# Kernel optimization log

Hardware: AMD Instinct MI355X
Metric: run time of the kernel (lower is better)

## Reference

```python
import jax, jax.numpy as jnp
import numpy as np
from jax import lax

N_FFT = 512
HOP = 128
Q = N_FFT // HOP  # 4
KW = 2 * N_FFT - 1  # conv kernel width 1023


def _hann_periodic(n: int) -> np.ndarray:
    # scipy.signal.get_window('hann', n) default fftbins=True -> periodic hann
    k = np.arange(n)
    return (0.5 - 0.5 * np.cos(2.0 * np.pi * k / n)).astype(np.float64)


def _compute_alpha(W: np.ndarray, S: np.ndarray) -> np.ndarray:
    # Faithful port of ConsistencyLoss._compute_alpha (paper eq. 9)
    N, R = N_FFT, HOP
    alpha = np.zeros((2 * Q - 1, 2 * N - 1), dtype=np.complex64)
    for qi, q in enumerate(range(-(Q - 1), Q)):
        S_sh = np.zeros(N)
        s0, s1 = max(0, -q * R), min(N, N - q * R)
        if s0 < s1:
            S_sh[s0:s1] = S[q * R + s0: q * R + s1]
        term = W * S_sh
        f = np.fft.fft(term, 2 * N - 1)
        alpha[qi] = np.fft.fftshift(f) / N
    alpha[Q - 1, N - 1] -= 1.0
    return alpha


def setup_inputs() -> dict:
    key = jax.random.key(0)
    waveform = 0.1 * jax.random.normal(key, (4, 131072), dtype=jnp.float32)
    W_np = _hann_periodic(N_FFT)
    alpha = _compute_alpha(W_np, W_np)
    return {
        "waveform": waveform,
        "window": jnp.asarray(W_np, dtype=jnp.float32),
        "alpha_real": jnp.asarray(alpha.real, dtype=jnp.float32),
        "alpha_imag": jnp.asarray(alpha.imag, dtype=jnp.float32),
    }


def _stft(waveform, window):
    # torch.stft(center=True, pad_mode='reflect', onesided=True), output (B, T, F)
    N, hop = N_FFT, HOP
    B, L = waveform.shape
    padded = jnp.pad(waveform, ((0, 0), (N // 2, N // 2)), mode="reflect")
    T = 1 + L // hop
    idx = hop * jnp.arange(T)[:, None] + jnp.arange(N)[None, :]  # (T, N)
    frames = padded[:, idx] * window  # (B, T, N)
    return jnp.fft.rfft(frames, axis=-1)  # (B, T, N//2+1) complex64


def reference(waveform, window, alpha_real, alpha_imag):
    N, hop = N_FFT, HOP
    B = waveform.shape[0]
    H = _stft(waveform, window)  # (B, T, N//2+1)
    T = H.shape[1]

    # reconstruct full two-sided spectrum: concat conj-flipped interior bins
    H_full = jnp.concatenate([H, jnp.conj(H[:, :, 1:-1][:, :, ::-1])], axis=2)  # (B, T, N)
    H_full = jnp.transpose(H_full, (0, 2, 1))  # (B, N, T)

    # fuse the phase-term einsum into the per-frequency conv kernel:
    # C[b,n,t] = sum_q phase[n,q] * (alpha[q] * H_full[b,n])(t)
    #          = (K_eff[n] * H_full[b,n])(t),  K_eff = phase @ alpha
    q_idx = jnp.arange(-(Q - 1), Q, dtype=jnp.float32)
    n_idx = jnp.arange(N, dtype=jnp.float32)
    phase = jnp.exp(1j * (2.0 * jnp.pi / N) * n_idx[:, None] * q_idx[None, :])  # (N, 2Q-1)
    alpha = alpha_real + 1j * alpha_imag  # (2Q-1, KW)
    K = phase @ alpha.astype(jnp.complex64)  # (N, KW)
    Kr, Ki = jnp.real(K), jnp.imag(K)

    # complex depthwise (groups=N) cross-correlation via real 2-channel trick
    Hri = jnp.stack([jnp.real(H_full), jnp.imag(H_full)], axis=2).reshape(B, 2 * N, T)
    kern = jnp.stack([
        jnp.stack([Kr, -Ki], axis=1),  # real output rows (N, 2, KW)
        jnp.stack([Ki, Kr], axis=1),   # imag output rows (N, 2, KW)
    ], axis=1).reshape(2 * N, 2, KW)
    out = lax.conv_general_dilated(
        Hri, kern, window_strides=(1,), padding=[(N - 1, N - 1)],
        dimension_numbers=("NCH", "OIH", "NCH"), feature_group_count=N,
    )  # (B, 2N, T)
    Cr, Ci = out[:, 0::2], out[:, 1::2]  # (B, N, T)

    loss = jnp.sum(Cr * Cr + Ci * Ci)
    return loss / (B * T)
```

## Files before the change

### kernel.cpp

```cpp
#include <hip/hip_runtime.h>
#include <math.h>

#define T_FRAMES 1025
#define TSTRIDE  1032
#define BATCH    4
#define LWAV     131072
#define KWC      1023
#define MFFT     2048
#define PI_F     3.14159265358979323846f

struct c32 { float r, i; };
__device__ __forceinline__ c32 mkc(float r, float i){ c32 z; z.r=r; z.i=i; return z; }
__device__ __forceinline__ c32 cadd(c32 a, c32 b){ return mkc(a.r+b.r, a.i+b.i); }
__device__ __forceinline__ c32 csub(c32 a, c32 b){ return mkc(a.r-b.r, a.i-b.i); }
__device__ __forceinline__ c32 cmul(c32 a, c32 b){ return mkc(a.r*b.r - a.i*b.i, a.r*b.i + a.i*b.r); }
__device__ __forceinline__ c32 cni(c32 a){ return mkc(a.i, -a.r); }
#define C8F 0.70710678118654752440f
__device__ __forceinline__ c32 c8p(c32 a){ return mkc(C8F*(a.r+a.i), C8F*(a.i-a.r)); }
__device__ __forceinline__ c32 c8m(c32 a){ return mkc(C8F*(a.i-a.r), -C8F*(a.r+a.i)); }

__device__ __forceinline__ int pX(int j){ return j + (j >> 5); }
__device__ __forceinline__ int pS(int j){ return j + (j >> 3); }

__device__ __forceinline__ c32 wexp(int r) {
    float s, c;
    __sincosf((float)r * (-PI_F / 1024.0f), &s, &c);
    return mkc(c, s);
}

__device__ __forceinline__ void dif8_tw(c32 y[8], c32 w3) {
    c32 w2 = cmul(w3, w3), w1 = cmul(w2, w2);
    c32 u[8], v[8], d;
    d = csub(y[0], y[4]); u[0] = cadd(y[0], y[4]); u[4] = cmul(d, w3);
    d = csub(y[1], y[5]); u[1] = cadd(y[1], y[5]); u[5] = c8p(cmul(d, w3));
    d = csub(y[2], y[6]); u[2] = cadd(y[2], y[6]); u[6] = cni(cmul(d, w3));
    d = csub(y[3], y[7]); u[3] = cadd(y[3], y[7]); u[7] = c8m(cmul(d, w3));
    d = csub(u[0], u[2]); v[0] = cadd(u[0], u[2]); v[2] = cmul(d, w2);
    d = csub(u[1], u[3]); v[1] = cadd(u[1], u[3]); v[3] = cni(cmul(d, w2));
    d = csub(u[4], u[6]); v[4] = cadd(u[4], u[6]); v[6] = cmul(d, w2);
    d = csub(u[5], u[7]); v[5] = cadd(u[5], u[7]); v[7] = cni(cmul(d, w2));
    d = csub(v[0], v[1]); y[0] = cadd(v[0], v[1]); y[1] = cmul(d, w1);
    d = csub(v[2], v[3]); y[2] = cadd(v[2], v[3]); y[3] = cmul(d, w1);
    d = csub(v[4], v[5]); y[4] = cadd(v[4], v[5]); y[5] = cmul(d, w1);
    d = csub(v[6], v[7]); y[6] = cadd(v[6], v[7]); y[7] = cmul(d, w1);
}
__device__ __forceinline__ void dif8_nt(c32 y[8]) {
    c32 u[8], v[8], d;
    d = csub(y[0], y[4]); u[0] = cadd(y[0], y[4]); u[4] = d;
    d = csub(y[1], y[5]); u[1] = cadd(y[1], y[5]); u[5] = c8p(d);
    d = csub(y[2], y[6]); u[2] = cadd(y[2], y[6]); u[6] = cni(d);
    d = csub(y[3], y[7]); u[3] = cadd(y[3], y[7]); u[7] = c8m(d);
    d = csub(u[0], u[2]); v[0] = cadd(u[0], u[2]); v[2] = d;
    d = csub(u[1], u[3]); v[1] = cadd(u[1], u[3]); v[3] = cni(d);
    d = csub(u[4], u[6]); v[4] = cadd(u[4], u[6]); v[6] = d;
    d = csub(u[5], u[7]); v[5] = cadd(u[5], u[7]); v[7] = cni(d);
    d = csub(v[0], v[1]); y[0] = cadd(v[0], v[1]); y[1] = d;
    d = csub(v[2], v[3]); y[2] = cadd(v[2], v[3]); y[3] = d;
    d = csub(v[4], v[5]); y[4] = cadd(v[4], v[5]); y[5] = d;
    d = csub(v[6], v[7]); y[6] = cadd(v[6], v[7]); y[7] = d;
}
__device__ __forceinline__ void dit8_tw(c32 y[8], c32 w3) {
    c32 w2 = cmul(w3, w3), w1 = cmul(w2, w2);
    c32 u[8], v[8], t;
    t = cmul(y[1], w1); u[0] = cadd(y[0], t); u[1] = csub(y[0], t);
    t = cmul(y[3], w1); u[2] = cadd(y[2], t); u[3] = csub(y[2], t);
    t = cmul(y[5], w1); u[4] = cadd(y[4], t); u[5] = csub(y[4], t);
    t = cmul(y[7], w1); u[6] = cadd(y[6], t); u[7] = csub(y[6], t);
    t = cmul(u[2], w2);      v[0] = cadd(u[0], t); v[2] = csub(u[0], t);
    t = cni(cmul(u[3], w2)); v[1] = cadd(u[1], t); v[3] = csub(u[1], t);
    t = cmul(u[6], w2);      v[4] = cadd(u[4], t); v[6] = csub(u[4], t);
    t = cni(cmul(u[7], w2)); v[5] = cadd(u[5], t); v[7] = csub(u[5], t);
    t = cmul(v[4], w3);      y[0] = cadd(v[0], t); y[4] = csub(v[0], t);
    t = c8p(cmul(v[5], w3)); y[1] = cadd(v[1], t); y[5] = csub(v[1], t);
    t = cni(cmul(v[6], w3)); y[2] = cadd(v[2], t); y[6] = csub(v[2], t);
    t = c8m(cmul(v[7], w3)); y[3] = cadd(v[3], t); y[7] = csub(v[3], t);
}
__device__ __forceinline__ void dit8_nt(c32 y[8]) {
    c32 u[8], v[8], t;
    u[0] = cadd(y[0], y[1]); u[1] = csub(y[0], y[1]);
    u[2] = cadd(y[2], y[3]); u[3] = csub(y[2], y[3]);
    u[4] = cadd(y[4], y[5]); u[5] = csub(y[4], y[5]);
    u[6] = cadd(y[6], y[7]); u[7] = csub(y[6], y[7]);
    t = u[2];      v[0] = cadd(u[0], t); v[2] = csub(u[0], t);
    t = cni(u[3]); v[1] = cadd(u[1], t); v[3] = csub(u[1], t);
    t = u[6];      v[4] = cadd(u[4], t); v[6] = csub(u[4], t);
    t = cni(u[7]); v[5] = cadd(u[5], t); v[7] = csub(u[5], t);
    t = v[4];      y[0] = cadd(v[0], t); y[4] = csub(v[0], t);
    t = c8p(v[5]); y[1] = cadd(v[1], t); y[5] = csub(v[1], t);
    t = cni(v[6]); y[2] = cadd(v[2], t); y[6] = csub(v[2], t);
    t = c8m(v[7]); y[3] = cadd(v[3], t); y[7] = csub(v[3], t);
}
__device__ __forceinline__ void dif4(c32 y[4]) {
    c32 u0 = cadd(y[0], y[2]), d0 = csub(y[0], y[2]);
    c32 u1 = cadd(y[1], y[3]), d1 = cni(csub(y[1], y[3]));
    y[0] = cadd(u0, u1); y[1] = csub(u0, u1);
    y[2] = cadd(d0, d1); y[3] = csub(d0, d1);
}
__device__ __forceinline__ void dit4(c32 y[4], c32 w) {
    c32 w2 = cmul(w, w);
    c32 t1 = cmul(y[1], w2); c32 u0 = cadd(y[0], t1), u1 = csub(y[0], t1);
    c32 t3 = cmul(y[3], w2); c32 u2 = cadd(y[2], t3), u3 = csub(y[2], t3);
    c32 s2 = cmul(u2, w);      y[0] = cadd(u0, s2); y[2] = csub(u0, s2);
    c32 s3 = cni(cmul(u3, w)); y[1] = cadd(u1, s3); y[3] = csub(u1, s3);
}

__global__ __launch_bounds__(256) void stage1_kernel(const float* __restrict__ wave,
                                                     const float* __restrict__ win,
                                                     const float* __restrict__ ar,
                                                     const float* __restrict__ ai,
                                                     float2* __restrict__ Ht,
                                                     float2* __restrict__ Afbr) {
    __shared__ float lds[9216];
    const int tid = threadIdx.x;

    if (blockIdx.x < 516) {
        float* Fr = lds;
        float* Fi = lds + 4608;
        const int w = tid >> 6, l = tid & 63;
        const int b = blockIdx.x / 129;
        const int t0 = (blockIdx.x - b * 129) << 3;
        const float* wb = wave + (size_t)b * LWAV;

        for (int pass = 0; pass < 2; ++pass) {
            const int j = w + (pass << 2);
            const int t = t0 + j;
            if (t < T_FRAMES) {
                c32 y[8];
#pragma unroll
                for (int k = 0; k < 8; ++k) {
                    int s = l + (k << 6);
                    int posn = t * 128 + s - 256;
                    int ix = posn < 0 ? -posn : (posn >= LWAV ? 2 * LWAV - 2 - posn : posn);
                    y[k] = mkc(wb[ix] * win[s], 0.f);
                }
                dif8_tw(y, wexp(l << 2));
#pragma unroll
                for (int k = 0; k < 8; ++k) { int p = pS(l + (k << 6)); Fr[j*576+p] = y[k].r; Fi[j*576+p] = y[k].i; }
                __builtin_amdgcn_wave_barrier();
                {
                    int base = ((l >> 3) << 6) + (l & 7);
#pragma unroll
                    for (int k = 0; k < 8; ++k) { int p = pS(base + (k << 3)); y[k] = mkc(Fr[j*576+p], Fi[j*576+p]); }
                    dif8_tw(y, wexp((l & 7) << 5));
#pragma unroll
                    for (int k = 0; k < 8; ++k) { int p = pS(base + (k << 3)); Fr[j*576+p] = y[k].r; Fi[j*576+p] = y[k].i; }
                }
                __builtin_amdgcn_wave_barrier();
                {
#pragma unroll
                    for (int k = 0; k < 8; ++k) { int p = pS((l << 3) + k); y[k] = mkc(Fr[j*576+p], Fi[j*576+p]); }
                    dif8_nt(y);
#pragma unroll
                    for (int k = 0; k < 8; ++k) { int p = pS((l << 3) + k); Fr[j*576+p] = y[k].r; Fi[j*576+p] = y[k].i; }
                }
            }
        }
        __syncthreads();
        const bool full = (t0 + 7 < T_FRAMES);
#pragma unroll
        for (int h = 0; h < 2; ++h) {
            int p = tid + (h << 8);
            int bin = (int)(__brev((unsigned)p) >> 23);
            if (bin > 256) continue;
            int ps = pS(p);
            size_t rowbase = (size_t)(b * 512 + p) * TSTRIDE + t0;
            if (full) {
                float4* dst = (float4*)(Ht + rowbase);
#pragma unroll
                for (int jj = 0; jj < 4; ++jj)
                    dst[jj] = make_float4(Fr[2*jj*576+ps], Fi[2*jj*576+ps], Fr[(2*jj+1)*576+ps], Fi[(2*jj+1)*576+ps]);
            } else {
                for (int jj = 0; jj < 8; ++jj)
                    if (t0 + jj < T_FRAMES) Ht[rowbase + jj] = make_float2(Fr[jj*576+ps], Fi[jj*576+ps]);
            }
        }
    } else {
        float* Xr = lds;
        float* Xi = lds + 2112;
        const int q = blockIdx.x - 516;
        c32 y[8];
#pragma unroll
        for (int k = 0; k < 8; ++k) {
            int j = tid + (k << 8);
            y[k] = (j < KWC) ? mkc(ar[q * KWC + j], -ai[q * KWC + j]) : mkc(0.f, 0.f);
        }
        dif8_tw(y, wexp(tid));
#pragma unroll
        for (int k = 0; k < 8; ++k) { int p = pX(tid + (k << 8)); Xr[p] = y[k].r; Xi[p] = y[k].i; }
        __syncthreads();
        {
            int base = ((tid >> 5) << 8) + (tid & 31);
#pragma unroll
            for (int k = 0; k < 8; ++k) { int p = pX(base + (k << 5)); y[k] = mkc(Xr[p], Xi[p]); }
            dif8_tw(y, wexp((tid & 31) << 3));
#pragma unroll
            for (int k = 0; k < 8; ++k) { int p = pX(base + (k << 5)); Xr[p] = y[k].r; Xi[p] = y[k].i; }
        }
        __syncthreads();
        {
            int base = ((tid & 63) << 5) + (tid >> 6);
#pragma unroll
            for (int k = 0; k < 8; ++k) { int p = pX(base + (k << 2)); y[k] = mkc(Xr[p], Xi[p]); }
            dif8_tw(y, wexp((tid >> 6) << 6));
#pragma unroll
            for (int k = 0; k < 8; ++k) { int p = pX(base + (k << 2)); Xr[p] = y[k].r; Xi[p] = y[k].i; }
        }
        __syncthreads();
#pragma unroll
        for (int h = 0; h < 2; ++h) {
            int g = tid + (h << 8);
            c32 z4[4];
#pragma unroll
            for (int k = 0; k < 4; ++k) { int p = pX((g << 2) + k); z4[k] = mkc(Xr[p], Xi[p]); }
            dif4(z4);
#pragma unroll
            for (int k = 0; k < 4; ++k) Afbr[(q << 11) + (g << 2) + k] = make_float2(z4[k].r, -z4[k].i);
        }
    }
}

__global__ __launch_bounds__(256) void conv_fft_kernel(const float2* __restrict__ Ht,
                                                       const float2* __restrict__ Afbr,
                                                       float* __restrict__ out) {
    __shared__ float Xr[2112], Xi[2112];
    __shared__ float red[4];
    const int tid = threadIdx.x;
    const int b = blockIdx.x / 257;
    const int n = blockIdx.x - b * 257;
    const int pr = (int)(__brev((unsigned)n) >> 23);

    const float2* row = Ht + (size_t)(b * 512 + pr) * TSTRIDE;
    c32 y[8];
#pragma unroll
    for (int k = 0; k < 8; ++k) {
        int j = tid + (k << 8);
        c32 v = mkc(0.f, 0.f);
        if (j < T_FRAMES) { float2 h = row[j]; v = mkc(h.x, h.y); }
        y[k] = v;
    }
    dif8_tw(y, wexp(tid));
#pragma unroll
    for (int k = 0; k < 8; ++k) { int p = pX(tid + (k << 8)); Xr[p] = y[k].r; Xi[p] = y[k].i; }
    __syncthreads();
    {
        int base = ((tid >> 5) << 8) + (tid & 31);
#pragma unroll
        for (int k = 0; k < 8; ++k) { int p = pX(base + (k << 5)); y[k] = mkc(Xr[p], Xi[p]); }
        dif8_tw(y, wexp((tid & 31) << 3));
#pragma unroll
        for (int k = 0; k < 8; ++k) { int p = pX(base + (k << 5)); Xr[p] = y[k].r; Xi[p] = y[k].i; }
    }
    __syncthreads();
    {
        int base = ((tid & 63) << 5) + (tid >> 6);
#pragma unroll
        for (int k = 0; k < 8; ++k) { int p = pX(base + (k << 2)); y[k] = mkc(Xr[p], Xi[p]); }
        dif8_tw(y, wexp((tid >> 6) << 6));
#pragma unroll
        for (int k = 0; k < 8; ++k) { int p = pX(base + (k << 2)); Xr[p] = y[k].r; Xi[p] = y[k].i; }
    }
    __syncthreads();
    {
        c32 p1 = wexp(-(n << 2));
        c32 p2 = cmul(p1, p1);
        c32 p3 = cmul(p2, p1);
        const int a0 = tid << 3;
        const int p0 = pX(a0);
        c32 z[8];
#pragma unroll
        for (int k = 0; k < 8; ++k) z[k] = mkc(Xr[p0 + k], Xi[p0 + k]);
        dif4(&z[0]);
        dif4(&z[4]);
        const float4* af4 = (const float4*)(Afbr + a0);
#pragma unroll
        for (int k = 0; k < 8; ++k) {
            float4 a;
            c32 Kk;
            a = af4[(3 << 10) + (k >> 1)];
            float ax = (k & 1) ? a.z : a.x, ay = (k & 1) ? a.w : a.y;
            Kk = mkc(ax, ay);
            a = af4[(4 << 10) + (k >> 1)]; ax = (k & 1) ? a.z : a.x; ay = (k & 1) ? a.w : a.y;
            Kk.r += p1.r * ax - p1.i * ay;  Kk.i += p1.r * ay + p1.i * ax;
            a = af4[(2 << 10) + (k >> 1)]; ax = (k & 1) ? a.z : a.x; ay = (k & 1) ? a.w : a.y;
            Kk.r += p1.r * ax + p1.i * ay;  Kk.i += p1.r * ay - p1.i * ax;
            a = af4[(5 << 10) + (k >> 1)]; ax = (k & 1) ? a.z : a.x; ay = (k & 1) ? a.w : a.y;
            Kk.r += p2.r * ax - p2.i * ay;  Kk.i += p2.r * ay + p2.i * ax;
            a = af4[(1 << 10) + (k >> 1)]; ax = (k & 1) ? a.z : a.x; ay = (k & 1) ? a.w : a.y;
            Kk.r += p2.r * ax + p2.i * ay;  Kk.i += p2.r * ay - p2.i * ax;
            a = af4[(6 << 10) + (k >> 1)]; ax = (k & 1) ? a.z : a.x; ay = (k & 1) ? a.w : a.y;
            Kk.r += p3.r * ax - p3.i * ay;  Kk.i += p3.r * ay + p3.i * ax;
            a = af4[(0 << 10) + (k >> 1)]; ax = (k & 1) ? a.z : a.x; ay = (k & 1) ? a.w : a.y;
            Kk.r += p3.r * ax + p3.i * ay;  Kk.i += p3.r * ay - p3.i * ax;
            c32 P = cmul(z[k], Kk);
            z[k] = mkc(P.r, -P.i);
        }
        dit8_nt(z);
#pragma unroll
        for (int k = 0; k < 8; ++k) { Xr[p0 + k] = z[k].r; Xi[p0 + k] = z[k].i; }
    }
    __syncthreads();
    {
        int G = (((tid & 63) >> 3) << 2) + (tid >> 6);
        int pos = tid & 7;
        int base = (G << 6) + pos;
#pragma unroll
        for (int k = 0; k < 8; ++k) { int p = pX(base + (k << 3)); y[k] = mkc(Xr[p], Xi[p]); }
        dit8_tw(y, wexp(pos << 5));
#pragma unroll
        for (int k = 0; k < 8; ++k) { int p = pX(base + (k << 3)); Xr[p] = y[k].r; Xi[p] = y[k].i; }
    }
    __syncthreads();
    {
        int base = ((tid >> 6) << 9) + (tid & 63);
#pragma unroll
        for (int k = 0; k < 8; ++k) { int p = pX(base + (k << 6)); y[k] = mkc(Xr[p], Xi[p]); }
        dit8_tw(y, wexp((tid & 63) << 2));
#pragma unroll
        for (int k = 0; k < 8; ++k) { int p = pX(base + (k << 6)); Xr[p] = y[k].r; Xi[p] = y[k].i; }
    }
    __syncthreads();
    float local = 0.f;
#pragma unroll
    for (int h = 0; h < 2; ++h) {
        int pos = tid + (h << 8);
        c32 z4[4];
#pragma unroll
        for (int k = 0; k < 4; ++k) { int p = pX(pos + (k << 9)); z4[k] = mkc(Xr[p], Xi[p]); }
        dit4(z4, wexp(pos));
        local += z4[0].r * z4[0].r + z4[0].i * z4[0].i;
        if (pos < 2)  local += z4[1].r * z4[1].r + z4[1].i * z4[1].i;
        if (pos >= 1) local += z4[3].r * z4[3].r + z4[3].i * z4[3].i;
    }
    local *= (n == 0 || n == 256) ? 1.0f : 2.0f;
#pragma unroll
    for (int off = 32; off >= 1; off >>= 1) local += __shfl_down(local, off);
    if ((tid & 63) == 0) red[tid >> 6] = local;
    __syncthreads();
    if (tid == 0) {
        const float SCALE =
            (float)(1.0 / ((double)MFFT * (double)MFFT * (double)BATCH * (double)T_FRAMES));
        atomicAdd(out, (red[0] + red[1] + red[2] + red[3]) * SCALE);
    }
}

extern "C" void kernel_launch(void* const* d_in, const int* in_sizes, int n_in,
                              void* d_out, int out_size, void* d_ws, size_t ws_size,
                              hipStream_t stream) {
    (void)in_sizes; (void)n_in; (void)out_size; (void)ws_size;
    const float* wave   = (const float*)d_in[0];
    const float* window = (const float*)d_in[1];
    const float* ar     = (const float*)d_in[2];
    const float* ai     = (const float*)d_in[3];
    float* out = (float*)d_out;

    char* ws = (char*)d_ws;
    float2* Ht   = (float2*)ws;
    float2* Afbr = (float2*)(ws + 16908288);

    hipMemsetAsync(out, 0, sizeof(float), stream);
    stage1_kernel<<<523, 256, 0, stream>>>(wave, window, ar, ai, Ht, Afbr);
    conv_fft_kernel<<<BATCH * 257, 256, 0, stream>>>(Ht, Afbr, out);
}
```

Baseline: 94.95 us.

## Run per-row conv FFT on a single wavefront and fold output zeroing into stage1

The per-frequency-row FFT convolution kernel now uses one 64-lane wavefront per row instead of four waves. Each lane handles four virtual threads, so the block-wide __syncthreads become wave barriers and the LDS cross-wave reduction goes away. Zeroing of the output scalar moves from a hipMemsetAsync into an extra stage1 block, which removes one launch. The trade-off is less parallelism per block and more serial work per lane, while the 1028 blocks stay the same.

```diff
diff --git a/kernel.cpp b/kernel.cpp
--- a/kernel.cpp
+++ b/kernel.cpp
@@ -21,6 +21,7 @@
 
 __device__ __forceinline__ int pX(int j){ return j + (j >> 5); }
 __device__ __forceinline__ int pS(int j){ return j + (j >> 3); }
+__device__ __forceinline__ int rev9(int j){ return (int)(__brev((unsigned)j) >> 23); }
 
 __device__ __forceinline__ c32 wexp(int r) {
     float s, c;
@@ -109,7 +110,8 @@
                                                      const float* __restrict__ ar,
                                                      const float* __restrict__ ai,
                                                      float2* __restrict__ Ht,
-                                                     float2* __restrict__ Afbr) {
+                                                     float2* __restrict__ Afbr,
+                                                     float* __restrict__ out) {
     __shared__ float lds[9216];
     const int tid = threadIdx.x;
 
@@ -160,7 +162,7 @@
 #pragma unroll
         for (int h = 0; h < 2; ++h) {
             int p = tid + (h << 8);
-            int bin = (int)(__brev((unsigned)p) >> 23);
+            int bin = rev9(p);
             if (bin > 256) continue;
             int ps = pS(p);
             size_t rowbase = (size_t)(b * 512 + p) * TSTRIDE + t0;
@@ -174,7 +176,7 @@
                     if (t0 + jj < T_FRAMES) Ht[rowbase + jj] = make_float2(Fr[jj*576+ps], Fi[jj*576+ps]);
             }
         }
-    } else {
+    } else if (blockIdx.x < 523) {
         float* Xr = lds;
         float* Xi = lds + 2112;
         const int q = blockIdx.x - 516;
@@ -216,113 +218,137 @@
 #pragma unroll
             for (int k = 0; k < 4; ++k) Afbr[(q << 11) + (g << 2) + k] = make_float2(z4[k].r, -z4[k].i);
         }
-    }
-}
-
-__global__ __launch_bounds__(256) void conv_fft_kernel(const float2* __restrict__ Ht,
-                                                       const float2* __restrict__ Afbr,
-                                                       float* __restrict__ out) {
-    __shared__ float Xr[2112], Xi[2112];
-    __shared__ float red[4];
-    const int tid = threadIdx.x;
-    const int b = blockIdx.x / 257;
-    const int n = blockIdx.x - b * 257;
-    const int pr = (int)(__brev((unsigned)n) >> 23);
+    } else {
+        if (tid == 0) *out = 0.f;
+    }
+}
+
+__global__ __launch_bounds__(64) void conv_kernel(const float2* __restrict__ Ht,
+                                                  const float2* __restrict__ Afbr,
+                                                  float* __restrict__ out) {
+    __shared__ float lds[4224];
+    const int l = threadIdx.x;
+    const int r = blockIdx.x;
+    const int b = r / 257;
+    const int n = r - b * 257;
+    const int pr = rev9(n);
+    float* Xr = lds;
+    float* Xi = lds + 2112;
 
     const float2* row = Ht + (size_t)(b * 512 + pr) * TSTRIDE;
-    c32 y[8];
-#pragma unroll
-    for (int k = 0; k < 8; ++k) {
-        int j = tid + (k << 8);
-        c32 v = mkc(0.f, 0.f);
-        if (j < T_FRAMES) { float2 h = row[j]; v = mkc(h.x, h.y); }
-        y[k] = v;
-    }
-    dif8_tw(y, wexp(tid));
-#pragma unroll
-    for (int k = 0; k < 8; ++k) { int p = pX(tid + (k << 8)); Xr[p] = y[k].r; Xi[p] = y[k].i; }
-    __syncthreads();
-    {
-        int base = ((tid >> 5) << 8) + (tid & 31);
+#pragma unroll
+    for (int u = 0; u < 4; ++u) {
+        int vt = l + (u << 6);
+        c32 y[8];
+#pragma unroll
+        for (int k = 0; k < 8; ++k) {
+            int j = vt + (k << 8);
+            c32 v = mkc(0.f, 0.f);
+            if (j < T_FRAMES) { float2 h = row[j]; v = mkc(h.x, h.y); }
+            y[k] = v;
+        }
+        dif8_tw(y, wexp(vt));
+#pragma unroll
+        for (int k = 0; k < 8; ++k) { int p = pX(vt + (k << 8)); Xr[p] = y[k].r; Xi[p] = y[k].i; }
+    }
+    __builtin_amdgcn_wave_barrier();
+#pragma unroll
+    for (int u = 0; u < 4; ++u) {
+        int vt = l + (u << 6);
+        int base = ((vt >> 5) << 8) + (vt & 31);
+        c32 y[8];
 #pragma unroll
         for (int k = 0; k < 8; ++k) { int p = pX(base + (k << 5)); y[k] = mkc(Xr[p], Xi[p]); }
-        dif8_tw(y, wexp((tid & 31) << 3));
+        dif8_tw(y, wexp((vt & 31) << 3));
 #pragma unroll
         for (int k = 0; k < 8; ++k) { int p = pX(base + (k << 5)); Xr[p] = y[k].r; Xi[p] = y[k].i; }
     }
-    __syncthreads();
-    {
-        int base = ((tid & 63) << 5) + (tid >> 6);
+    __builtin_amdgcn_wave_barrier();
+#pragma unroll
+    for (int u = 0; u < 4; ++u) {
+        int vt = l + (u << 6);
+        int base = ((vt & 63) << 5) + (vt >> 6);
+        c32 y[8];
 #pragma unroll
         for (int k = 0; k < 8; ++k) { int p = pX(base + (k << 2)); y[k] = mkc(Xr[p], Xi[p]); }
-        dif8_tw(y, wexp((tid >> 6) << 6));
+        dif8_tw(y, wexp((vt >> 6) << 6));
 #pragma unroll
         for (int k = 0; k < 8; ++k) { int p = pX(base + (k << 2)); Xr[p] = y[k].r; Xi[p] = y[k].i; }
     }
-    __syncthreads();
+    __builtin_amdgcn_wave_barrier();
     {
         c32 p1 = wexp(-(n << 2));
         c32 p2 = cmul(p1, p1);
         c32 p3 = cmul(p2, p1);
-        const int a0 = tid << 3;
-        const int p0 = pX(a0);
-        c32 z[8];
-#pragma unroll
-        for (int k = 0; k < 8; ++k) z[k] = mkc(Xr[p0 + k], Xi[p0 + k]);
-        dif4(&z[0]);
-        dif4(&z[4]);
-        const float4* af4 = (const float4*)(Afbr + a0);
-#pragma unroll
-        for (int k = 0; k < 8; ++k) {
-            float4 a;
-            c32 Kk;
-            a = af4[(3 << 10) + (k >> 1)];
-            float ax = (k & 1) ? a.z : a.x, ay = (k & 1) ? a.w : a.y;
-            Kk = mkc(ax, ay);
-            a = af4[(4 << 10) + (k >> 1)]; ax = (k & 1) ? a.z : a.x; ay = (k & 1) ? a.w : a.y;
-            Kk.r += p1.r * ax - p1.i * ay;  Kk.i += p1.r * ay + p1.i * ax;
-            a = af4[(2 << 10) + (k >> 1)]; ax = (k & 1) ? a.z : a.x; ay = (k & 1) ? a.w : a.y;
-            Kk.r += p1.r * ax + p1.i * ay;  Kk.i += p1.r * ay - p1.i * ax;
-            a = af4[(5 << 10) + (k >> 1)]; ax = (k & 1) ? a.z : a.x; ay = (k & 1) ? a.w : a.y;
-            Kk.r += p2.r * ax - p2.i * ay;  Kk.i += p2.r * ay + p2.i * ax;
-            a = af4[(1 << 10) + (k >> 1)]; ax = (k & 1) ? a.z : a.x; ay = (k & 1) ? a.w : a.y;
-            Kk.r += p2.r * ax + p2.i * ay;  Kk.i += p2.r * ay - p2.i * ax;
-            a = af4[(6 << 10) + (k >> 1)]; ax = (k & 1) ? a.z : a.x; ay = (k & 1) ? a.w : a.y;
-            Kk.r += p3.r * ax - p3.i * ay;  Kk.i += p3.r * ay + p3.i * ax;
-            a = af4[(0 << 10) + (k >> 1)]; ax = (k & 1) ? a.z : a.x; ay = (k & 1) ? a.w : a.y;
-            Kk.r += p3.r * ax + p3.i * ay;  Kk.i += p3.r * ay - p3.i * ax;
-            c32 P = cmul(z[k], Kk);
-            z[k] = mkc(P.r, -P.i);
-        }
-        dit8_nt(z);
-#pragma unroll
-        for (int k = 0; k < 8; ++k) { Xr[p0 + k] = z[k].r; Xi[p0 + k] = z[k].i; }
-    }
-    __syncthreads();
-    {
-        int G = (((tid & 63) >> 3) << 2) + (tid >> 6);
-        int pos = tid & 7;
+#pragma unroll
+        for (int u = 0; u < 4; ++u) {
+            int vt = l + (u << 6);
+            const int a0 = vt << 3;
+            const int p0 = pX(a0);
+            c32 z[8];
+#pragma unroll
+            for (int k = 0; k < 8; ++k) z[k] = mkc(Xr[p0 + k], Xi[p0 + k]);
+            dif4(&z[0]);
+            dif4(&z[4]);
+            const float4* af4 = (const float4*)(Afbr + a0);
+#pragma unroll
+            for (int k = 0; k < 8; ++k) {
+                float4 a;
+                c32 Kk;
+                a = af4[(3 << 10) + (k >> 1)];
+                float ax = (k & 1) ? a.z : a.x, ay = (k & 1) ? a.w : a.y;
+                Kk = mkc(ax, ay);
+                a = af4[(4 << 10) + (k >> 1)]; ax = (k & 1) ? a.z : a.x; ay = (k & 1) ? a.w : a.y;
+                Kk.r += p1.r * ax - p1.i * ay;  Kk.i += p1.r * ay + p1.i * ax;
+                a = af4[(2 << 10) + (k >> 1)]; ax = (k & 1) ? a.z : a.x; ay = (k & 1) ? a.w : a.y;
+                Kk.r += p1.r * ax + p1.i * ay;  Kk.i += p1.r * ay - p1.i * ax;
+                a = af4[(5 << 10) + (k >> 1)]; ax = (k & 1) ? a.z : a.x; ay = (k & 1) ? a.w : a.y;
+                Kk.r += p2.r * ax - p2.i * ay;  Kk.i += p2.r * ay + p2.i * ax;
+                a = af4[(1 << 10) + (k >> 1)]; ax = (k & 1) ? a.z : a.x; ay = (k & 1) ? a.w : a.y;
+                Kk.r += p2.r * ax + p2.i * ay;  Kk.i += p2.r * ay - p2.i * ax;
+                a = af4[(6 << 10) + (k >> 1)]; ax = (k & 1) ? a.z : a.x; ay = (k & 1) ? a.w : a.y;
+                Kk.r += p3.r * ax - p3.i * ay;  Kk.i += p3.r * ay + p3.i * ax;
+                a = af4[(0 << 10) + (k >> 1)]; ax = (k & 1) ? a.z : a.x; ay = (k & 1) ? a.w : a.y;
+                Kk.r += p3.r * ax + p3.i * ay;  Kk.i += p3.r * ay - p3.i * ax;
+                c32 P = cmul(z[k], Kk);
+                z[k] = mkc(P.r, -P.i);
+            }
+            dit8_nt(z);
+#pragma unroll
+            for (int k = 0; k < 8; ++k) { Xr[p0 + k] = z[k].r; Xi[p0 + k] = z[k].i; }
+        }
+    }
+    __builtin_amdgcn_wave_barrier();
+#pragma unroll
+    for (int u = 0; u < 4; ++u) {
+        int vt = l + (u << 6);
+        int G = (((vt & 63) >> 3) << 2) + (vt >> 6);
+        int pos = vt & 7;
         int base = (G << 6) + pos;
+        c32 y[8];
 #pragma unroll
         for (int k = 0; k < 8; ++k) { int p = pX(base + (k << 3)); y[k] = mkc(Xr[p], Xi[p]); }
         dit8_tw(y, wexp(pos << 5));
 #pragma unroll
         for (int k = 0; k < 8; ++k) { int p = pX(base + (k << 3)); Xr[p] = y[k].r; Xi[p] = y[k].i; }
     }
-    __syncthreads();
-    {
-        int base = ((tid >> 6) << 9) + (tid & 63);
+    __builtin_amdgcn_wave_barrier();
+#pragma unroll
+    for (int u = 0; u < 4; ++u) {
+        int vt = l + (u << 6);
+        int base = ((vt >> 6) << 9) + (vt & 63);
+        c32 y[8];
 #pragma unroll
         for (int k = 0; k < 8; ++k) { int p = pX(base + (k << 6)); y[k] = mkc(Xr[p], Xi[p]); }
-        dit8_tw(y, wexp((tid & 63) << 2));
+        dit8_tw(y, wexp((vt & 63) << 2));
 #pragma unroll
         for (int k = 0; k < 8; ++k) { int p = pX(base + (k << 6)); Xr[p] = y[k].r; Xi[p] = y[k].i; }
     }
-    __syncthreads();
+    __builtin_amdgcn_wave_barrier();
     float local = 0.f;
 #pragma unroll
-    for (int h = 0; h < 2; ++h) {
-        int pos = tid + (h << 8);
+    for (int v = 0; v < 8; ++v) {
+        int pos = l + (v << 6);
         c32 z4[4];
 #pragma unroll
         for (int k = 0; k < 4; ++k) { int p = pX(pos + (k << 9)); z4[k] = mkc(Xr[p], Xi[p]); }
@@ -334,12 +360,10 @@
     local *= (n == 0 || n == 256) ? 1.0f : 2.0f;
 #pragma unroll
     for (int off = 32; off >= 1; off >>= 1) local += __shfl_down(local, off);
-    if ((tid & 63) == 0) red[tid >> 6] = local;
-    __syncthreads();
-    if (tid == 0) {
+    if (l == 0) {
         const float SCALE =
             (float)(1.0 / ((double)MFFT * (double)MFFT * (double)BATCH * (double)T_FRAMES));
-        atomicAdd(out, (red[0] + red[1] + red[2] + red[3]) * SCALE);
+        atomicAdd(out, local * SCALE);
     }
 }
 
@@ -357,7 +381,6 @@
     float2* Ht   = (float2*)ws;
     float2* Afbr = (float2*)(ws + 16908288);
 
-    hipMemsetAsync(out, 0, sizeof(float), stream);
-    stage1_kernel<<<523, 256, 0, stream>>>(wave, window, ar, ai, Ht, Afbr);
-    conv_fft_kernel<<<BATCH * 257, 256, 0, stream>>>(Ht, Afbr, out);
-}
+    stage1_kernel<<<524, 256, 0, stream>>>(wave, window, ar, ai, Ht, Afbr, out);
+    conv_kernel<<<BATCH * 257, 64, 0, stream>>>(Ht, Afbr, out);
+}
```

Measured after the change: 110.2 us. 1.16x slower.

## Process two batches per conv block sharing kernel spectrum; fold memset into stage1

Applied to the files above, without the earlier changes.

The convolution kernel now handles two batch rows of the same frequency bin per block. The effective kernel spectrum Kk is built once and applied to both, and twiddle computation is shared across the two FFTs, which halves the Afbr reloads and phase math and halves the block count. The host memset is replaced by an extra stage1 block that zeroes the output, removing one launch. The cost is doubled LDS and register use per block, which can lower occupancy, plus fewer blocks (514) to spread across CUs.

```diff
diff --git a/kernel.cpp b/kernel.cpp
--- a/kernel.cpp
+++ b/kernel.cpp
@@ -21,6 +21,7 @@
 
 __device__ __forceinline__ int pX(int j){ return j + (j >> 5); }
 __device__ __forceinline__ int pS(int j){ return j + (j >> 3); }
+__device__ __forceinline__ int rev9(int j){ return (int)(__brev((unsigned)j) >> 23); }
 
 __device__ __forceinline__ c32 wexp(int r) {
     float s, c;
@@ -109,7 +110,8 @@
                                                      const float* __restrict__ ar,
                                                      const float* __restrict__ ai,
                                                      float2* __restrict__ Ht,
-                                                     float2* __restrict__ Afbr) {
+                                                     float2* __restrict__ Afbr,
+                                                     float* __restrict__ out) {
     __shared__ float lds[9216];
     const int tid = threadIdx.x;
 
@@ -160,7 +162,7 @@
 #pragma unroll
         for (int h = 0; h < 2; ++h) {
             int p = tid + (h << 8);
-            int bin = (int)(__brev((unsigned)p) >> 23);
+            int bin = rev9(p);
             if (bin > 256) continue;
             int ps = pS(p);
             size_t rowbase = (size_t)(b * 512 + p) * TSTRIDE + t0;
@@ -174,7 +176,7 @@
                     if (t0 + jj < T_FRAMES) Ht[rowbase + jj] = make_float2(Fr[jj*576+ps], Fi[jj*576+ps]);
             }
         }
-    } else {
+    } else if (blockIdx.x < 523) {
         float* Xr = lds;
         float* Xi = lds + 2112;
         const int q = blockIdx.x - 516;
@@ -216,48 +218,89 @@
 #pragma unroll
             for (int k = 0; k < 4; ++k) Afbr[(q << 11) + (g << 2) + k] = make_float2(z4[k].r, -z4[k].i);
         }
-    }
-}
-
-__global__ __launch_bounds__(256) void conv_fft_kernel(const float2* __restrict__ Ht,
-                                                       const float2* __restrict__ Afbr,
-                                                       float* __restrict__ out) {
-    __shared__ float Xr[2112], Xi[2112];
-    __shared__ float red[4];
+    } else {
+        if (tid == 0) *out = 0.f;
+    }
+}
+
+__global__ __launch_bounds__(256) void conv_kernel(const float2* __restrict__ Ht,
+                                                   const float2* __restrict__ Afbr,
+                                                   float* __restrict__ out) {
+    __shared__ float lds[8452];
+    float* X0r = lds;
+    float* X0i = lds + 2112;
+    float* X1r = lds + 4224;
+    float* X1i = lds + 6336;
+    float* red = lds + 8448;
     const int tid = threadIdx.x;
-    const int b = blockIdx.x / 257;
-    const int n = blockIdx.x - b * 257;
-    const int pr = (int)(__brev((unsigned)n) >> 23);
-
-    const float2* row = Ht + (size_t)(b * 512 + pr) * TSTRIDE;
-    c32 y[8];
+    const int g = blockIdx.x;
+    const int half = g / 257;
+    const int n = g - half * 257;
+    const int b0 = half << 1;
+    const int pr = rev9(n);
+
+    const float2* row0 = Ht + (size_t)(b0 * 512 + pr) * TSTRIDE;
+    const float2* row1 = Ht + (size_t)((b0 + 1) * 512 + pr) * TSTRIDE;
+
+    c32 y0[8], y1[8];
 #pragma unroll
     for (int k = 0; k < 8; ++k) {
         int j = tid + (k << 8);
-        c32 v = mkc(0.f, 0.f);
-        if (j < T_FRAMES) { float2 h = row[j]; v = mkc(h.x, h.y); }
-        y[k] = v;
-    }
-    dif8_tw(y, wexp(tid));
-#pragma unroll
-    for (int k = 0; k < 8; ++k) { int p = pX(tid + (k << 8)); Xr[p] = y[k].r; Xi[p] = y[k].i; }
+        c32 v0 = mkc(0.f, 0.f), v1 = mkc(0.f, 0.f);
+        if (j < T_FRAMES) {
+            float2 h0 = row0[j]; v0 = mkc(h0.x, h0.y);
+            float2 h1 = row1[j]; v1 = mkc(h1.x, h1.y);
+        }
+        y0[k] = v0; y1[k] = v1;
+    }
+    {
+        c32 w3 = wexp(tid);
+        dif8_tw(y0, w3);
+        dif8_tw(y1, w3);
+#pragma unroll
+        for (int k = 0; k < 8; ++k) {
+            int p = pX(tid + (k << 8));
+            X0r[p] = y0[k].r; X0i[p] = y0[k].i;
+            X1r[p] = y1[k].r; X1i[p] = y1[k].i;
+        }
+    }
     __syncthreads();
     {
         int base = ((tid >> 5) << 8) + (tid & 31);
 #pragma unroll
-        for (int k = 0; k < 8; ++k) { int p = pX(base + (k << 5)); y[k] = mkc(Xr[p], Xi[p]); }
-        dif8_tw(y, wexp((tid & 31) << 3));
-#pragma unroll
-        for (int k = 0; k < 8; ++k) { int p = pX(base + (k << 5)); Xr[p] = y[k].r; Xi[p] = y[k].i; }
+        for (int k = 0; k < 8; ++k) {
+            int p = pX(base + (k << 5));
+            y0[k] = mkc(X0r[p], X0i[p]);
+            y1[k] = mkc(X1r[p], X1i[p]);
+        }
+        c32 w3 = wexp((tid & 31) << 3);
+        dif8_tw(y0, w3);
+        dif8_tw(y1, w3);
+#pragma unroll
+        for (int k = 0; k < 8; ++k) {
+            int p = pX(base + (k << 5));
+            X0r[p] = y0[k].r; X0i[p] = y0[k].i;
+            X1r[p] = y1[k].r; X1i[p] = y1[k].i;
+        }
     }
     __syncthreads();
     {
         int base = ((tid & 63) << 5) + (tid >> 6);
 #pragma unroll
-        for (int k = 0; k < 8; ++k) { int p = pX(base + (k << 2)); y[k] = mkc(Xr[p], Xi[p]); }
-        dif8_tw(y, wexp((tid >> 6) << 6));
-#pragma unroll
-        for (int k = 0; k < 8; ++k) { int p = pX(base + (k << 2)); Xr[p] = y[k].r; Xi[p] = y[k].i; }
+        for (int k = 0; k < 8; ++k) {
+            int p = pX(base + (k << 2));
+            y0[k] = mkc(X0r[p], X0i[p]);
+            y1[k] = mkc(X1r[p], X1i[p]);
+        }
+        c32 w3 = wexp((tid >> 6) << 6);
+        dif8_tw(y0, w3);
+        dif8_tw(y1, w3);
+#pragma unroll
+        for (int k = 0; k < 8; ++k) {
+            int p = pX(base + (k << 2));
+            X0r[p] = y0[k].r; X0i[p] = y0[k].i;
+            X1r[p] = y1[k].r; X1i[p] = y1[k].i;
+        }
     }
     __syncthreads();
     {
@@ -266,11 +309,13 @@
         c32 p3 = cmul(p2, p1);
         const int a0 = tid << 3;
         const int p0 = pX(a0);
-        c32 z[8];
-#pragma unroll
-        for (int k = 0; k < 8; ++k) z[k] = mkc(Xr[p0 + k], Xi[p0 + k]);
-        dif4(&z[0]);
-        dif4(&z[4]);
+#pragma unroll
+        for (int k = 0; k < 8; ++k) {
+            y0[k] = mkc(X0r[p0 + k], X0i[p0 + k]);
+            y1[k] = mkc(X1r[p0 + k], X1i[p0 + k]);
+        }
+        dif4(&y0[0]); dif4(&y0[4]);
+        dif4(&y1[0]); dif4(&y1[4]);
         const float4* af4 = (const float4*)(Afbr + a0);
 #pragma unroll
         for (int k = 0; k < 8; ++k) {
@@ -291,12 +336,18 @@
             Kk.r += p3.r * ax - p3.i * ay;  Kk.i += p3.r * ay + p3.i * ax;
             a = af4[(0 << 10) + (k >> 1)]; ax = (k & 1) ? a.z : a.x; ay = (k & 1) ? a.w : a.y;
             Kk.r += p3.r * ax + p3.i * ay;  Kk.i += p3.r * ay - p3.i * ax;
-            c32 P = cmul(z[k], Kk);
-            z[k] = mkc(P.r, -P.i);
-        }
-        dit8_nt(z);
-#pragma unroll
-        for (int k = 0; k < 8; ++k) { Xr[p0 + k] = z[k].r; Xi[p0 + k] = z[k].i; }
+            c32 P0 = cmul(y0[k], Kk);
+            c32 P1 = cmul(y1[k], Kk);
+            y0[k] = mkc(P0.r, -P0.i);
+            y1[k] = mkc(P1.r, -P1.i);
+        }
+        dit8_nt(y0);
+        dit8_nt(y1);
+#pragma unroll
+        for (int k = 0; k < 8; ++k) {
+            X0r[p0 + k] = y0[k].r; X0i[p0 + k] = y0[k].i;
+            X1r[p0 + k] = y1[k].r; X1i[p0 + k] = y1[k].i;
+        }
     }
     __syncthreads();
     {
@@ -304,32 +355,61 @@
         int pos = tid & 7;
         int base = (G << 6) + pos;
 #pragma unroll
-        for (int k = 0; k < 8; ++k) { int p = pX(base + (k << 3)); y[k] = mkc(Xr[p], Xi[p]); }
-        dit8_tw(y, wexp(pos << 5));
-#pragma unroll
-        for (int k = 0; k < 8; ++k) { int p = pX(base + (k << 3)); Xr[p] = y[k].r; Xi[p] = y[k].i; }
+        for (int k = 0; k < 8; ++k) {
+            int p = pX(base + (k << 3));
+            y0[k] = mkc(X0r[p], X0i[p]);
+            y1[k] = mkc(X1r[p], X1i[p]);
+        }
+        c32 w3 = wexp(pos << 5);
+        dit8_tw(y0, w3);
+        dit8_tw(y1, w3);
+#pragma unroll
+        for (int k = 0; k < 8; ++k) {
+            int p = pX(base + (k << 3));
+            X0r[p] = y0[k].r; X0i[p] = y0[k].i;
+            X1r[p] = y1[k].r; X1i[p] = y1[k].i;
+        }
     }
     __syncthreads();
     {
         int base = ((tid >> 6) << 9) + (tid & 63);
 #pragma unroll
-        for (int k = 0; k < 8; ++k) { int p = pX(base + (k << 6)); y[k] = mkc(Xr[p], Xi[p]); }
-        dit8_tw(y, wexp((tid & 63) << 2));
-#pragma unroll
-        for (int k = 0; k < 8; ++k) { int p = pX(base + (k << 6)); Xr[p] = y[k].r; Xi[p] = y[k].i; }
+        for (int k = 0; k < 8; ++k) {
+            int p = pX(base + (k << 6));
+            y0[k] = mkc(X0r[p], X0i[p]);
+            y1[k] = mkc(X1r[p], X1i[p]);
+        }
+        c32 w3 = wexp((tid & 63) << 2);
+        dit8_tw(y0, w3);
+        dit8_tw(y1, w3);
+#pragma unroll
+        for (int k = 0; k < 8; ++k) {
+            int p = pX(base + (k << 6));
+            X0r[p] = y0[k].r; X0i[p] = y0[k].i;
+            X1r[p] = y1[k].r; X1i[p] = y1[k].i;
+        }
     }
     __syncthreads();
     float local = 0.f;
 #pragma unroll
     for (int h = 0; h < 2; ++h) {
         int pos = tid + (h << 8);
-        c32 z4[4];
-#pragma unroll
-        for (int k = 0; k < 4; ++k) { int p = pX(pos + (k << 9)); z4[k] = mkc(Xr[p], Xi[p]); }
-        dit4(z4, wexp(pos));
-        local += z4[0].r * z4[0].r + z4[0].i * z4[0].i;
-        if (pos < 2)  local += z4[1].r * z4[1].r + z4[1].i * z4[1].i;
-        if (pos >= 1) local += z4[3].r * z4[3].r + z4[3].i * z4[3].i;
+        c32 w = wexp(pos);
+        c32 z0[4], z1[4];
+#pragma unroll
+        for (int k = 0; k < 4; ++k) {
+            int p = pX(pos + (k << 9));
+            z0[k] = mkc(X0r[p], X0i[p]);
+            z1[k] = mkc(X1r[p], X1i[p]);
+        }
+        dit4(z0, w);
+        dit4(z1, w);
+        local += z0[0].r * z0[0].r + z0[0].i * z0[0].i
+               + z1[0].r * z1[0].r + z1[0].i * z1[0].i;
+        if (pos < 2)  local += z0[1].r * z0[1].r + z0[1].i * z0[1].i
+                             + z1[1].r * z1[1].r + z1[1].i * z1[1].i;
+        if (pos >= 1) local += z0[3].r * z0[3].r + z0[3].i * z0[3].i
+                             + z1[3].r * z1[3].r + z1[3].i * z1[3].i;
     }
     local *= (n == 0 || n == 256) ? 1.0f : 2.0f;
 #pragma unroll
@@ -357,7 +437,6 @@
     float2* Ht   = (float2*)ws;
     float2* Afbr = (float2*)(ws + 16908288);
 
-    hipMemsetAsync(out, 0, sizeof(float), stream);
-    stage1_kernel<<<523, 256, 0, stream>>>(wave, window, ar, ai, Ht, Afbr);
-    conv_fft_kernel<<<BATCH * 257, 256, 0, stream>>>(Ht, Afbr, out);
-}
+    stage1_kernel<<<524, 256, 0, stream>>>(wave, window, ar, ai, Ht, Afbr, out);
+    conv_kernel<<<2 * 257, 256, 0, stream>>>(Ht, Afbr, out);
+}
```

Measured after the change: 86.55 us (median of 2 runs). 8.8% less time.
